# Performance work log

Hardware: AMD Instinct MI355X
Metric: run time of the kernel (lower is better)

Reference implementation:

```python
import jax, jax.numpy as jnp
import numpy as np

N_AGENTS, BATCH, SEQ, HID = 256, 64, 20, 128
RADIUS = 0.15


def setup_inputs() -> dict:
    key = jax.random.key(0)
    k1, k2 = jax.random.split(key)
    agent_hidden_states = jax.random.normal(k1, (N_AGENTS, BATCH, SEQ, HID), dtype=jnp.float32)
    agent_positions = jax.random.uniform(k2, (N_AGENTS, BATCH, SEQ, 2), dtype=jnp.float32)
    radius = jnp.float32(RADIUS)
    return {"agent_hidden_states": agent_hidden_states,
            "agent_positions": agent_positions,
            "radius": radius}


def reference(agent_hidden_states, agent_positions, radius):
    # pool_type == 'mean': for each target agent i, average the last-step hidden
    # states of all other agents j whose last-step position is within `radius`.
    h_last = agent_hidden_states[:, :, -1, :]      # [N, B, H]
    p_last = agent_positions[:, :, -1, :]          # [N, B, 2]
    N = h_last.shape[0]
    # pairwise last-step distances: [N_target, N_neighbor, B]
    diff = p_last[:, None, :, :] - p_last[None, :, :, :]
    dist = jnp.sqrt(jnp.sum(diff * diff, axis=-1))
    within = (dist <= radius) & (~jnp.eye(N, dtype=bool))[:, :, None]  # exclude self
    m = within.astype(h_last.dtype)                # [N, N, B]
    # masked sum of neighbor hiddens, divided by neighbor count (clamped to 1)
    ctx_sum = jnp.einsum('ijb,jbh->ibh', m, h_last)       # [N, B, H]
    count = jnp.clip(jnp.sum(m, axis=1), 1.0)             # [N, B]
    return ctx_sum / count[..., None]
```

## Files before the change

### kernel.cpp

```cpp
#include <hip/hip_runtime.h>

constexpr int NA = 256;
constexpr int B  = 64;
constexpr int S  = 20;
constexpr int H  = 128;

constexpr int AGENTS_PER_BLOCK = 16;
constexpr int BLOCKS = (NA / AGENTS_PER_BLOCK) * B;

__global__ __launch_bounds__(256, 4) void social_pool_kernel(
    const float* __restrict__ h,
    const float* __restrict__ p,
    const float* __restrict__ rptr,
    float* __restrict__ out)
{
    const int group = blockIdx.x & (NA / AGENTS_PER_BLOCK - 1);
    const int b     = blockIdx.x >> 4;
    const int tid   = threadIdx.x;
    const int wave  = tid >> 6;
    const int lane  = tid & 63;

    __shared__ float px[NA];
    __shared__ float py[NA];

    {
        const int j = tid;
        const float2 pj = *(const float2*)(p + (((size_t)(j * B + b)) * S + (S - 1)) * 2);
        px[j] = pj.x;
        py[j] = pj.y;
    }
    __syncthreads();

    const float r = *rptr;

    const size_t jstride = (size_t)B * S * H;
    const float* hb = h + ((size_t)b * S + (S - 1)) * H + 2 * lane;

    for (int a = 0; a < 4; ++a) {
        const int i = group * AGENTS_PER_BLOCK + wave * 4 + a;
        const float xi = px[i];
        const float yi = py[i];

        unsigned long long m[4];
        #pragma unroll
        for (int k = 0; k < 4; ++k) {
            const int j = (k << 6) + lane;
            const float dx   = __fsub_rn(xi, px[j]);
            const float dy   = __fsub_rn(yi, py[j]);
            const float d2   = __fadd_rn(__fmul_rn(dx, dx), __fmul_rn(dy, dy));
            const float dist = __fsqrt_rn(d2);
            m[k] = __ballot(dist <= r);
        }
        m[i >> 6] &= ~(1ull << (i & 63));

        const int n = __popcll(m[0]) + __popcll(m[1]) + __popcll(m[2]) + __popcll(m[3]);

        float ax = 0.0f, ay = 0.0f;
        while (m[0] | m[1] | m[2] | m[3]) {
            float2 v[4];
            bool got[4];
            #pragma unroll
            for (int k = 0; k < 4; ++k) {
                got[k] = (m[k] != 0ull);
                if (got[k]) {
                    const int j = (k << 6) + __builtin_ctzll(m[k]);
                    m[k] &= m[k] - 1ull;
                    v[k] = *(const float2*)(hb + (size_t)j * jstride);
                }
            }
            #pragma unroll
            for (int k = 0; k < 4; ++k) {
                if (got[k]) { ax += v[k].x; ay += v[k].y; }
            }
        }

        const float c = (float)(n > 0 ? n : 1);
        float2 o;
        o.x = __fdiv_rn(ax, c);
        o.y = __fdiv_rn(ay, c);
        *(float2*)(out + ((size_t)i * B + b) * H + 2 * lane) = o;
    }
}

extern "C" void kernel_launch(void* const* d_in, const int* in_sizes, int n_in,
                              void* d_out, int out_size, void* d_ws, size_t ws_size,
                              hipStream_t stream) {
    const float* h    = (const float*)d_in[0];
    const float* p    = (const float*)d_in[1];
    const float* rptr = (const float*)d_in[2];
    float* out        = (float*)d_out;

    (void)in_sizes; (void)n_in; (void)out_size; (void)d_ws; (void)ws_size;

    social_pool_kernel<<<dim3(BLOCKS), dim3(256), 0, stream>>>(h, p, rptr, out);
}
```

Measured before the change: 217.5 us.

## Stage all neighbor hidden rows in LDS and process 64 targets per block

Each 1024-thread block now handles 64 target agents for one batch. It copies all 256 last-step hidden rows for that batch into a 128KB shared-memory buffer, in four chunks. The next chunk is prefetched into registers while the current one is consumed. Neighbor accumulation reads from LDS instead of doing scattered global float2 loads per neighbor, and the batch index is swizzled across blocks. The cost is that each batch's hidden rows are loaded four times (once per target group), and the large LDS footprint limits residency to one block per CU with only 256 blocks in the grid.

```diff
diff --git a/kernel.cpp b/kernel.cpp
--- a/kernel.cpp
+++ b/kernel.cpp
@@ -5,43 +5,51 @@
 constexpr int S  = 20;
 constexpr int H  = 128;
 
-constexpr int AGENTS_PER_BLOCK = 16;
-constexpr int BLOCKS = (NA / AGENTS_PER_BLOCK) * B;
-
-__global__ __launch_bounds__(256, 4) void social_pool_kernel(
+__global__ __launch_bounds__(1024, 4) void social_pool_kernel(
     const float* __restrict__ h,
     const float* __restrict__ p,
     const float* __restrict__ rptr,
     float* __restrict__ out)
 {
-    const int group = blockIdx.x & (NA / AGENTS_PER_BLOCK - 1);
-    const int b     = blockIdx.x >> 4;
+    const int bid   = blockIdx.x;
+    const int inner = bid & 63;
+    const int b     = ((inner & 7) << 3) | (inner >> 3);
+    const int ic    = bid >> 6;
     const int tid   = threadIdx.x;
     const int wave  = tid >> 6;
     const int lane  = tid & 63;
 
+    __shared__ float hs[NA * H];
     __shared__ float px[NA];
     __shared__ float py[NA];
 
-    {
-        const int j = tid;
-        const float2 pj = *(const float2*)(p + (((size_t)(j * B + b)) * S + (S - 1)) * 2);
-        px[j] = pj.x;
-        py[j] = pj.y;
+    if (tid < NA) {
+        const float2 pj = *(const float2*)(p + (((size_t)(tid * B + b)) * S + (S - 1)) * 2);
+        px[tid] = pj.x;
+        py[tid] = pj.y;
     }
     __syncthreads();
 
     const float r = *rptr;
 
-    const size_t jstride = (size_t)B * S * H;
-    const float* hb = h + ((size_t)b * S + (S - 1)) * H + 2 * lane;
+    const int colf = (lane & 31) << 2;
+    const int rsub = (wave << 2) + (lane >> 5);
+    const size_t jstr = (size_t)B * S * H;
+    const size_t boff = (size_t)b * S * H + (size_t)(S - 1) * H;
 
+    auto gsrc = [&](int j) -> const float4* {
+        return (const float4*)(h + (size_t)j * jstr + boff + colf);
+    };
+
+    float4 ra = *gsrc(rsub);
+    float4 rb = *gsrc(rsub + 2);
+
+    const int i0 = (ic << 6) + (wave << 2);
+    unsigned long long m[4][4];
+    #pragma unroll
     for (int a = 0; a < 4; ++a) {
-        const int i = group * AGENTS_PER_BLOCK + wave * 4 + a;
-        const float xi = px[i];
-        const float yi = py[i];
-
-        unsigned long long m[4];
+        const float xi = px[i0 + a];
+        const float yi = py[i0 + a];
         #pragma unroll
         for (int k = 0; k < 4; ++k) {
             const int j = (k << 6) + lane;
@@ -49,36 +57,57 @@
             const float dy   = __fsub_rn(yi, py[j]);
             const float d2   = __fadd_rn(__fmul_rn(dx, dx), __fmul_rn(dy, dy));
             const float dist = __fsqrt_rn(d2);
-            m[k] = __ballot(dist <= r);
+            m[a][k] = __ballot(dist <= r);
+            if (k == ic) m[a][k] &= ~(1ull << ((i0 + a) & 63));
         }
-        m[i >> 6] &= ~(1ull << (i & 63));
+    }
+    int n[4];
+    #pragma unroll
+    for (int a = 0; a < 4; ++a)
+        n[a] = __popcll(m[a][0]) + __popcll(m[a][1]) + __popcll(m[a][2]) + __popcll(m[a][3]);
 
-        const int n = __popcll(m[0]) + __popcll(m[1]) + __popcll(m[2]) + __popcll(m[3]);
+    const int lo2 = lane << 1;
+    float ax[4] = {0.f, 0.f, 0.f, 0.f};
+    float ay[4] = {0.f, 0.f, 0.f, 0.f};
 
-        float ax = 0.0f, ay = 0.0f;
-        while (m[0] | m[1] | m[2] | m[3]) {
-            float2 v[4];
-            bool got[4];
-            #pragma unroll
-            for (int k = 0; k < 4; ++k) {
-                got[k] = (m[k] != 0ull);
-                if (got[k]) {
-                    const int j = (k << 6) + __builtin_ctzll(m[k]);
-                    m[k] &= m[k] - 1ull;
-                    v[k] = *(const float2*)(hb + (size_t)j * jstride);
-                }
-            }
-            #pragma unroll
-            for (int k = 0; k < 4; ++k) {
-                if (got[k]) { ax += v[k].x; ay += v[k].y; }
-            }
+    #pragma unroll
+    for (int c = 0; c < 4; ++c) {
+        {
+            const int j0 = (c << 6) + rsub;
+            *(float4*)(hs + j0 * H + colf)       = ra;
+            *(float4*)(hs + (j0 + 2) * H + colf) = rb;
+        }
+        __syncthreads();
+        if (c < 3) {
+            const int j0 = ((c + 1) << 6) + rsub;
+            ra = *gsrc(j0);
+            rb = *gsrc(j0 + 2);
         }
 
-        const float c = (float)(n > 0 ? n : 1);
+        unsigned long long g0 = m[0][c], g1 = m[1][c], g2 = m[2][c], g3 = m[3][c];
+        const float* base = hs + (c << 6) * H + lo2;
+        while (g0 | g1 | g2 | g3) {
+            float2 v0, v1, v2, v3;
+            const bool h0 = g0 != 0ull, h1 = g1 != 0ull, h2 = g2 != 0ull, h3 = g3 != 0ull;
+            if (h0) { const int j = __builtin_ctzll(g0); g0 &= g0 - 1ull; v0 = *(const float2*)(base + j * H); }
+            if (h1) { const int j = __builtin_ctzll(g1); g1 &= g1 - 1ull; v1 = *(const float2*)(base + j * H); }
+            if (h2) { const int j = __builtin_ctzll(g2); g2 &= g2 - 1ull; v2 = *(const float2*)(base + j * H); }
+            if (h3) { const int j = __builtin_ctzll(g3); g3 &= g3 - 1ull; v3 = *(const float2*)(base + j * H); }
+            if (h0) { ax[0] += v0.x; ay[0] += v0.y; }
+            if (h1) { ax[1] += v1.x; ay[1] += v1.y; }
+            if (h2) { ax[2] += v2.x; ay[2] += v2.y; }
+            if (h3) { ax[3] += v3.x; ay[3] += v3.y; }
+        }
+    }
+
+    #pragma unroll
+    for (int a = 0; a < 4; ++a) {
+        const int i = i0 + a;
+        const float cnt = (float)(n[a] > 0 ? n[a] : 1);
         float2 o;
-        o.x = __fdiv_rn(ax, c);
-        o.y = __fdiv_rn(ay, c);
-        *(float2*)(out + ((size_t)i * B + b) * H + 2 * lane) = o;
+        o.x = __fdiv_rn(ax[a], cnt);
+        o.y = __fdiv_rn(ay[a], cnt);
+        *(float2*)(out + ((size_t)i * B + b) * H + lo2) = o;
     }
 }
 
@@ -92,5 +121,6 @@
 
     (void)in_sizes; (void)n_in; (void)out_size; (void)d_ws; (void)ws_size;
 
-    social_pool_kernel<<<dim3(BLOCKS), dim3(256), 0, stream>>>(h, p, rptr, out);
+    constexpr int BLOCKS = B * (NA / 64);
+    social_pool_kernel<<<dim3(BLOCKS), dim3(1024), 0, stream>>>(h, p, rptr, out);
 }
```

Measured after the change: 212.3 us. 2.4% less time.
